# Performance work log

Measured on AMD Instinct MI355X. Metric: run time of the kernel, lower is better.

The kernel has to match this reference:

```python
import jax, jax.numpy as jnp
import numpy as np

NCLASSES = 1000
K = 5
REG_STRENGTH = 1.0


def isotonic_l2(y):
    """Solve min_v 0.5||v - y||^2 s.t. v_1 >= v_2 >= ... >= v_n, per row.

    Uses the exact min-max characterization of isotonic regression:
      sol_i = min_{j<=i} max_{k>=i} mean(y[j..k])
    (equivalent to pool-adjacent-violators), fully vectorized.
    y: [B, n] -> [B, n]
    """
    b, n = y.shape
    cs = jnp.concatenate([jnp.zeros((b, 1), y.dtype), jnp.cumsum(y, axis=-1)], axis=-1)  # [B, n+1]
    j = jnp.arange(n)[:, None]  # block start
    k = jnp.arange(n)[None, :]  # block end
    length = (k - j + 1).astype(y.dtype)
    # M[b, j, k] = mean(y[b, j..k]) for k >= j, else -inf (ignored by the max)
    M = (cs[:, None, 1:] - cs[:, :-1, None]) / jnp.where(k >= j, length, 1.0)
    M = jnp.where(k >= j, M, -jnp.inf)
    A = jax.lax.cummax(M, axis=2, reverse=True)  # A[b, j, i] = max_{k>=i} M[b, j, k]
    A = jnp.where(j <= k, A, jnp.inf)            # restrict min to j <= i
    return jnp.min(A, axis=1)                     # [B, n]


def soft_rank(values, strength):
    """torchsort.soft_rank with l2 regularization.

    r = theta - sigma^{-1}(isotonic_l2(sort_desc(theta) - w)),  theta = values/strength,
    w = [n, n-1, ..., 1].  Larger values get larger (soft) ranks.
    """
    n = values.shape[-1]
    theta = values / strength
    perm = jnp.argsort(-theta, axis=-1)                 # descending order
    s = jnp.take_along_axis(theta, perm, axis=-1)
    inv_perm = jnp.argsort(perm, axis=-1)
    w = jnp.arange(n, 0, -1, dtype=values.dtype)
    sol = isotonic_l2(s - w[None, :])
    return jnp.take_along_axis(s - sol, inv_perm, axis=-1)


def setup_inputs() -> dict:
    key = jax.random.key(0)
    k1, k2 = jax.random.split(key)
    output = jax.random.normal(k1, (64, NCLASSES), dtype=jnp.float32)
    target = jax.random.randint(k2, (64,), 0, NCLASSES, dtype=jnp.int32)
    return {"output": output, "target": target}


def reference(output, target):
    ranks = soft_rank(output, REG_STRENGTH)                              # [B, n]
    ranks_label = jnp.take_along_axis(ranks, target[:, None], axis=-1)   # [B, 1]
    return jnp.mean(jax.nn.relu(NCLASSES - ranks_label - K + 1))
```

## Files before the change

kernel.cpp:

```cpp
#include <hip/hip_runtime.h>
#include <math.h>

#define N     1000
#define NPAD  1024
#define NTH1  512
#define NTH2  256
#define MSLICE 16
#define SROW  1040
#define META  (64 * SROW)

__device__ inline unsigned fkey(float x) {
    unsigned u = __float_as_uint(x);
    return (u & 0x80000000u) ? ~u : (u | 0x80000000u);
}
__device__ inline float fdecode(unsigned u) {
    return __uint_as_float((u & 0x80000000u) ? (u & 0x7FFFFFFFu) : ~u);
}

__global__ __launch_bounds__(NTH1) void k1_sort_scan(
    const float* __restrict__ mat, const int* __restrict__ target,
    float* __restrict__ ws)
{
    __shared__ float sx[NPAD];
    __shared__ float wtot[8];
    __shared__ int   cnt_sh;

    const int tid  = threadIdx.x;
    const int lane = tid & 63;
    const int w    = tid >> 6;
    const int i0   = (w << 7) + lane;
    const int i1   = i0 + 64;
    const int r    = blockIdx.x;
    const float* row = mat + r * N;
    const int   tgt  = target[r];
    const float tval = row[tgt];

    float r0 = row[i0];
    float r1 = (i1 < N) ? row[i1] : -INFINITY;
    if (tid == 0) cnt_sh = 0;

    int lc = ((r0 > tval) || (r0 == tval && i0 < tgt))
           + ((r1 > tval) || (r1 == tval && i1 < tgt));
    #pragma unroll
    for (int off = 32; off; off >>= 1) lc += __shfl_down(lc, off);
    __syncthreads();
    if (lane == 0 && lc) atomicAdd(&cnt_sh, lc);

    auto cas_shfl = [&](float& rr, int i, unsigned k, unsigned j) {
        float o = __shfl_xor(rr, (int)j);
        bool lower = ((lane & (int)j) == 0);
        bool desc  = ((i & (int)k) == 0);
        rr = (lower == desc) ? fmaxf(rr, o) : fminf(rr, o);
    };
    #pragma unroll
    for (unsigned k = 2; k <= 64; k <<= 1)
        #pragma unroll
        for (unsigned j = k >> 1; j; j >>= 1) { cas_shfl(r0, i0, k, j); cas_shfl(r1, i1, k, j); }
    #pragma unroll
    for (unsigned k = 128; k <= 1024; k <<= 1) {
        #pragma unroll
        for (unsigned j = k >> 1; j >= 128; j >>= 1) {
            __syncthreads();
            sx[i0] = r0; sx[i1] = r1;
            __syncthreads();
            float o0 = sx[i0 ^ (int)j], o1 = sx[i1 ^ (int)j];
            bool lower = ((i0 & (int)j) == 0);
            bool desc  = ((i0 & (int)k) == 0);
            r0 = (lower == desc) ? fmaxf(r0, o0) : fminf(r0, o0);
            r1 = (lower == desc) ? fmaxf(r1, o1) : fminf(r1, o1);
        }
        {
            bool desc = ((i0 & (int)k) == 0);
            float a = fmaxf(r0, r1), b = fminf(r0, r1);
            r0 = desc ? a : b;
            r1 = desc ? b : a;
        }
        #pragma unroll
        for (unsigned j = 32; j; j >>= 1) { cas_shfl(r0, i0, k, j); cas_shfl(r1, i1, k, j); }
    }

    if (i1 >= N) r1 = 0.0f;
    float incl0 = r0;
    #pragma unroll
    for (int off = 1; off < 64; off <<= 1) {
        float y = __shfl_up(incl0, off);
        if (lane >= off) incl0 += y;
    }
    float tot0 = __shfl(incl0, 63);
    float incl1 = r1;
    #pragma unroll
    for (int off = 1; off < 64; off <<= 1) {
        float y = __shfl_up(incl1, off);
        if (lane >= off) incl1 += y;
    }
    if (lane == 63) wtot[w] = incl0 + incl1;
    __syncthreads();
    float base = 0.0f;
    #pragma unroll
    for (int u = 0; u < 8; ++u) { float t = wtot[u]; if (u < w) base += t; }

    float* Sg = ws + r * SROW;
    if (tid == 0) Sg[0] = 0.0f;
    Sg[i0 + 1] = base + incl0;
    Sg[i1 + 1] = base + tot0 + incl1;
    if (tid == 0) {
        ((int*)ws)[META + r]            = cnt_sh;
        ws[META + 64 + r]               = tval;
        ((unsigned*)ws)[META + 128 + r] = 0xFFFFFFFFu;
    }
}

__global__ __launch_bounds__(NTH2) void k2_minmax(
    const float* __restrict__ Sg, const int* __restrict__ pw,
    unsigned* __restrict__ mr)
{
    __shared__ float Sloc[N];
    __shared__ float rtab[N];
    __shared__ float maxh[NTH2];

    const int r  = blockIdx.y;
    const int m  = blockIdx.x;
    const int t  = threadIdx.x;
    const int p  = pw[r];
    const int j0 = m * 64;
    if (j0 > p) return;
    const int len = N - p;
    const float* Srow = Sg + r * SROW;

    const int jl = t & 63;
    const int j  = j0 + jl;
    const float Sj = (j <= p) ? Srow[j] : 0.0f;

    for (int i = t; i < len; i += NTH2) Sloc[i] = Srow[p + 1 + i];
    for (int d = t; d < N; d += NTH2) rtab[d] = 1.0f / (float)(d + 1);
    __syncthreads();

    const int q  = t >> 6;
    const int k0 = (q * len) >> 2;
    const int k1 = ((q + 1) * len) >> 2;
    float maxv = -INFINITY;
    if (j <= p) {
        const float* sp = &Sloc[k0];
        const float* rp = &rtab[p + k0 - j];
        float c = 0.5f * (float)(j + p + k0) - (float)N;
        #pragma unroll 8
        for (int it = 0; it < k1 - k0; ++it) {
            float mval = fmaf(sp[it] - Sj, rp[it], c);
            maxv = fmaxf(maxv, mval);
            c += 0.5f;
        }
    }
    maxh[t] = maxv;
    __syncthreads();
    if (t < 64) {
        float mv = fmaxf(fmaxf(maxh[t], maxh[t + 64]),
                         fmaxf(maxh[t + 128], maxh[t + 192]));
        float minv = (j0 + t <= p) ? mv : INFINITY;
        #pragma unroll
        for (int off = 32; off; off >>= 1)
            minv = fminf(minv, __shfl_down(minv, off));
        if (t == 0) atomicMin(&mr[r], fkey(minv));
    }
}

__global__ __launch_bounds__(64) void k3_loss(
    const unsigned* __restrict__ mr, const float* __restrict__ tv,
    float* __restrict__ out, int nrows)
{
    int t = threadIdx.x;
    float loss = 0.0f;
    if (t < nrows) {
        float sol  = fdecode(mr[t]);
        float rank = tv[t] - sol;
        loss = fmaxf(0.0f, (float)(N - 5 + 1) - rank);
    }
    #pragma unroll
    for (int off = 32; off; off >>= 1) loss += __shfl_down(loss, off);
    if (t == 0) out[0] = loss / (float)nrows;
}

__global__ __launch_bounds__(NTH1) void topk_loss_mono(
    const float* __restrict__ mat, const int* __restrict__ target,
    float* __restrict__ d_out, int nrows)
{
    __shared__ float S[NPAD + 1];
    __shared__ float rcp[N];
    __shared__ float sx[NPAD];
    __shared__ float wtot[8];
    __shared__ float red[8];
    __shared__ int   cnt_sh;

    const int tid  = threadIdx.x;
    const int lane = tid & 63;
    const int w    = tid >> 6;
    const int i0   = (w << 7) + lane;
    const int i1   = i0 + 64;
    const float* row = mat + blockIdx.x * N;
    const int   tgt  = target[blockIdx.x];
    const float tval = row[tgt];

    float r0 = row[i0];
    float r1 = (i1 < N) ? row[i1] : -INFINITY;
    if (tid == 0) cnt_sh = 0;
    rcp[tid] = 1.0f / (float)(tid + 1);
    if (tid + NTH1 < N) rcp[tid + NTH1] = 1.0f / (float)(tid + NTH1 + 1);

    int lc = ((r0 > tval) || (r0 == tval && i0 < tgt))
           + ((r1 > tval) || (r1 == tval && i1 < tgt));
    #pragma unroll
    for (int off = 32; off; off >>= 1) lc += __shfl_down(lc, off);
    __syncthreads();
    if (lane == 0 && lc) atomicAdd(&cnt_sh, lc);

    auto cas_shfl = [&](float& rr, int i, unsigned k, unsigned j) {
        float o = __shfl_xor(rr, (int)j);
        bool lower = ((lane & (int)j) == 0);
        bool desc  = ((i & (int)k) == 0);
        rr = (lower == desc) ? fmaxf(rr, o) : fminf(rr, o);
    };
    #pragma unroll
    for (unsigned k = 2; k <= 64; k <<= 1)
        #pragma unroll
        for (unsigned j = k >> 1; j; j >>= 1) { cas_shfl(r0, i0, k, j); cas_shfl(r1, i1, k, j); }
    #pragma unroll
    for (unsigned k = 128; k <= 1024; k <<= 1) {
        #pragma unroll
        for (unsigned j = k >> 1; j >= 128; j >>= 1) {
            __syncthreads();
            sx[i0] = r0; sx[i1] = r1;
            __syncthreads();
            float o0 = sx[i0 ^ (int)j], o1 = sx[i1 ^ (int)j];
            bool lower = ((i0 & (int)j) == 0);
            bool desc  = ((i0 & (int)k) == 0);
            r0 = (lower == desc) ? fmaxf(r0, o0) : fminf(r0, o0);
            r1 = (lower == desc) ? fmaxf(r1, o1) : fminf(r1, o1);
        }
        {
            bool desc = ((i0 & (int)k) == 0);
            float a = fmaxf(r0, r1), b = fminf(r0, r1);
            r0 = desc ? a : b;
            r1 = desc ? b : a;
        }
        #pragma unroll
        for (unsigned j = 32; j; j >>= 1) { cas_shfl(r0, i0, k, j); cas_shfl(r1, i1, k, j); }
    }

    if (i1 >= N) r1 = 0.0f;
    float incl0 = r0;
    #pragma unroll
    for (int off = 1; off < 64; off <<= 1) {
        float y = __shfl_up(incl0, off);
        if (lane >= off) incl0 += y;
    }
    float tot0 = __shfl(incl0, 63);
    float incl1 = r1;
    #pragma unroll
    for (int off = 1; off < 64; off <<= 1) {
        float y = __shfl_up(incl1, off);
        if (lane >= off) incl1 += y;
    }
    if (lane == 63) wtot[w] = incl0 + incl1;
    __syncthreads();
    float base = 0.0f;
    #pragma unroll
    for (int u = 0; u < 8; ++u) { float t = wtot[u]; if (u < w) base += t; }
    if (tid == 0) S[0] = 0.0f;
    S[i0 + 1] = base + incl0;
    S[i1 + 1] = base + tot0 + incl1;
    __syncthreads();

    const int p   = cnt_sh;
    const int len = N - p;
    float minv = INFINITY;
    for (int j = tid; j <= p; j += NTH1) {
        const float  Sj = S[j];
        const float* Sp = &S[p + 1];
        const float* rp = &rcp[p - j];
        const float  cj = 0.5f * (float)(j + p) - (float)N;
        float maxv = -INFINITY;
        #pragma unroll 8
        for (int it = 0; it < len; ++it) {
            float mm = fmaf(Sp[it] - Sj, rp[it], cj + 0.5f * (float)it);
            maxv = fmaxf(maxv, mm);
        }
        minv = fminf(minv, maxv);
    }
    #pragma unroll
    for (int off = 32; off; off >>= 1) minv = fminf(minv, __shfl_down(minv, off));
    if (lane == 0) red[w] = minv;
    __syncthreads();
    if (tid == 0) {
        float sol = red[0];
        #pragma unroll
        for (int u = 1; u < 8; ++u) sol = fminf(sol, red[u]);
        float rank_label = tval - sol;
        float loss = fmaxf(0.0f, (float)(N - 5 + 1) - rank_label);
        atomicAdd(d_out, loss / (float)nrows);
    }
}

extern "C" void kernel_launch(void* const* d_in, const int* in_sizes, int n_in,
                              void* d_out, int out_size, void* d_ws, size_t ws_size,
                              hipStream_t stream) {
    (void)n_in;
    const float* mat    = (const float*)d_in[0];
    const int*   target = (const int*)d_in[1];
    float*       out    = (float*)d_out;
    const int    nrows  = in_sizes[1];

    const size_t need = (size_t)(META + 192) * sizeof(float);
    if (nrows == 64 && ws_size >= need) {
        float*    ws = (float*)d_ws;
        float*    Sg = ws;
        int*      pw = (int*)(ws + META);
        float*    tv = ws + META + 64;
        unsigned* mr = (unsigned*)(ws + META + 128);
        k1_sort_scan<<<nrows, NTH1, 0, stream>>>(mat, target, ws);
        dim3 g2(MSLICE, nrows);
        k2_minmax<<<g2, NTH2, 0, stream>>>(Sg, pw, mr);
        k3_loss<<<1, 64, 0, stream>>>(mr, tv, out, nrows);
    } else {
        hipMemsetAsync(out, 0, sizeof(float) * out_size, stream);
        topk_loss_mono<<<nrows, NTH1, 0, stream>>>(mat, target, out, nrows);
    }
}
```

Baseline: 70.31 us.

## Fuse final loss kernel into minmax via last-block atomic counter; double-buffer sort

Removes the third kernel launch. The final loss reduction now runs in whichever k2 block is last to increment a global done-counter, which k1 resets. The block-wide bitonic stages in k1 use a double-buffered shared array, cutting one __syncthreads per stage. This trades a launch and a barrier per stage for an extra atomic and a threadfence in every k2 block.

```diff
diff --git a/kernel.cpp b/kernel.cpp
--- a/kernel.cpp
+++ b/kernel.cpp
@@ -1,13 +1,13 @@
 #include <hip/hip_runtime.h>
 #include <math.h>
 
-#define N     1000
-#define NPAD  1024
-#define NTH1  512
-#define NTH2  256
+#define N      1000
+#define NTH1   512
+#define NTH2   256
 #define MSLICE 16
-#define SROW  1040
-#define META  (64 * SROW)
+#define SROW   1008
+#define META   (64 * SROW)
+#define K2_BLOCKS (MSLICE * 64)
 
 __device__ inline unsigned fkey(float x) {
     unsigned u = __float_as_uint(x);
@@ -21,7 +21,7 @@
     const float* __restrict__ mat, const int* __restrict__ target,
     float* __restrict__ ws)
 {
-    __shared__ float sx[NPAD];
+    __shared__ float sx[2][1024];
     __shared__ float wtot[8];
     __shared__ int   cnt_sh;
 
@@ -56,14 +56,15 @@
     for (unsigned k = 2; k <= 64; k <<= 1)
         #pragma unroll
         for (unsigned j = k >> 1; j; j >>= 1) { cas_shfl(r0, i0, k, j); cas_shfl(r1, i1, k, j); }
+    int buf = 0;
     #pragma unroll
     for (unsigned k = 128; k <= 1024; k <<= 1) {
         #pragma unroll
         for (unsigned j = k >> 1; j >= 128; j >>= 1) {
+            sx[buf][i0] = r0; sx[buf][i1] = r1;
             __syncthreads();
-            sx[i0] = r0; sx[i1] = r1;
-            __syncthreads();
-            float o0 = sx[i0 ^ (int)j], o1 = sx[i1 ^ (int)j];
+            float o0 = sx[buf][i0 ^ (int)j], o1 = sx[buf][i1 ^ (int)j];
+            buf ^= 1;
             bool lower = ((i0 & (int)j) == 0);
             bool desc  = ((i0 & (int)k) == 0);
             r0 = (lower == desc) ? fmaxf(r0, o0) : fminf(r0, o0);
@@ -102,90 +103,92 @@
     float* Sg = ws + r * SROW;
     if (tid == 0) Sg[0] = 0.0f;
     Sg[i0 + 1] = base + incl0;
-    Sg[i1 + 1] = base + tot0 + incl1;
+    if (i1 < N) Sg[i1 + 1] = base + tot0 + incl1;
     if (tid == 0) {
         ((int*)ws)[META + r]            = cnt_sh;
         ws[META + 64 + r]               = tval;
         ((unsigned*)ws)[META + 128 + r] = 0xFFFFFFFFu;
+        if (r == 0) ((unsigned*)ws)[META + 192] = 0u;
     }
 }
 
 __global__ __launch_bounds__(NTH2) void k2_minmax(
-    const float* __restrict__ Sg, const int* __restrict__ pw,
-    unsigned* __restrict__ mr)
+    float* __restrict__ ws, float* __restrict__ out)
 {
     __shared__ float Sloc[N];
     __shared__ float rtab[N];
     __shared__ float maxh[NTH2];
+    __shared__ int   amLast;
 
     const int r  = blockIdx.y;
     const int m  = blockIdx.x;
     const int t  = threadIdx.x;
-    const int p  = pw[r];
+    const int p  = ((const int*)ws)[META + r];
     const int j0 = m * 64;
-    if (j0 > p) return;
-    const int len = N - p;
-    const float* Srow = Sg + r * SROW;
-
-    const int jl = t & 63;
-    const int j  = j0 + jl;
-    const float Sj = (j <= p) ? Srow[j] : 0.0f;
-
-    for (int i = t; i < len; i += NTH2) Sloc[i] = Srow[p + 1 + i];
-    for (int d = t; d < N; d += NTH2) rtab[d] = 1.0f / (float)(d + 1);
-    __syncthreads();
-
-    const int q  = t >> 6;
-    const int k0 = (q * len) >> 2;
-    const int k1 = ((q + 1) * len) >> 2;
-    float maxv = -INFINITY;
-    if (j <= p) {
-        const float* sp = &Sloc[k0];
-        const float* rp = &rtab[p + k0 - j];
-        float c = 0.5f * (float)(j + p + k0) - (float)N;
-        #pragma unroll 8
-        for (int it = 0; it < k1 - k0; ++it) {
-            float mval = fmaf(sp[it] - Sj, rp[it], c);
-            maxv = fmaxf(maxv, mval);
-            c += 0.5f;
-        }
-    }
-    maxh[t] = maxv;
-    __syncthreads();
-    if (t < 64) {
-        float mv = fmaxf(fmaxf(maxh[t], maxh[t + 64]),
-                         fmaxf(maxh[t + 128], maxh[t + 192]));
-        float minv = (j0 + t <= p) ? mv : INFINITY;
-        #pragma unroll
-        for (int off = 32; off; off >>= 1)
-            minv = fminf(minv, __shfl_down(minv, off));
-        if (t == 0) atomicMin(&mr[r], fkey(minv));
-    }
-}
-
-__global__ __launch_bounds__(64) void k3_loss(
-    const unsigned* __restrict__ mr, const float* __restrict__ tv,
-    float* __restrict__ out, int nrows)
-{
-    int t = threadIdx.x;
-    float loss = 0.0f;
-    if (t < nrows) {
-        float sol  = fdecode(mr[t]);
-        float rank = tv[t] - sol;
-        loss = fmaxf(0.0f, (float)(N - 5 + 1) - rank);
-    }
-    #pragma unroll
-    for (int off = 32; off; off >>= 1) loss += __shfl_down(loss, off);
-    if (t == 0) out[0] = loss / (float)nrows;
+    unsigned* mr   = (unsigned*)ws + META + 128;
+    unsigned* done = (unsigned*)ws + META + 192;
+
+    if (j0 <= p) {
+        const int len = N - p;
+        const float* Srow = ws + r * SROW;
+        const int jl = t & 63;
+        const int j  = j0 + jl;
+        const float Sj = (j <= p) ? Srow[j] : 0.0f;
+
+        for (int i = t; i < len; i += NTH2) Sloc[i] = Srow[p + 1 + i];
+        for (int d = t; d < N; d += NTH2) rtab[d] = 1.0f / (float)(d + 1);
+        __syncthreads();
+
+        const int q  = t >> 6;
+        const int k0 = (q * len) >> 2;
+        const int k1 = ((q + 1) * len) >> 2;
+        float maxv = -INFINITY;
+        if (j <= p) {
+            const float* sp = &Sloc[k0];
+            const float* rp = &rtab[p + k0 - j];
+            float c = 0.5f * (float)(j + p + k0) - (float)N;
+            #pragma unroll 8
+            for (int it = 0; it < k1 - k0; ++it) {
+                float mval = fmaf(sp[it] - Sj, rp[it], c);
+                maxv = fmaxf(maxv, mval);
+                c += 0.5f;
+            }
+        }
+        maxh[t] = maxv;
+        __syncthreads();
+        if (t < 64) {
+            float mv = fmaxf(fmaxf(maxh[t], maxh[t + 64]),
+                             fmaxf(maxh[t + 128], maxh[t + 192]));
+            float minv = (j0 + t <= p) ? mv : INFINITY;
+            #pragma unroll
+            for (int off = 32; off; off >>= 1)
+                minv = fminf(minv, __shfl_down(minv, off));
+            if (t == 0) atomicMin(&mr[r], fkey(minv));
+        }
+    }
+
+    if (t == 0) {
+        __threadfence();
+        amLast = (atomicAdd(done, 1u) == K2_BLOCKS - 1);
+    }
+    __syncthreads();
+    if (amLast && t < 64) {
+        float sol  = fdecode(atomicAdd(&mr[t], 0u));
+        float tval = ws[META + 64 + t];
+        float loss = fmaxf(0.0f, (float)(N - 5 + 1) - (tval - sol));
+        #pragma unroll
+        for (int off = 32; off; off >>= 1) loss += __shfl_down(loss, off);
+        if (t == 0) out[0] = loss / 64.0f;
+    }
 }
 
 __global__ __launch_bounds__(NTH1) void topk_loss_mono(
     const float* __restrict__ mat, const int* __restrict__ target,
     float* __restrict__ d_out, int nrows)
 {
-    __shared__ float S[NPAD + 1];
+    __shared__ float S[1025];
     __shared__ float rcp[N];
-    __shared__ float sx[NPAD];
+    __shared__ float sx[1024];
     __shared__ float wtot[8];
     __shared__ float red[8];
     __shared__ int   cnt_sh;
@@ -308,17 +311,12 @@
     float*       out    = (float*)d_out;
     const int    nrows  = in_sizes[1];
 
-    const size_t need = (size_t)(META + 192) * sizeof(float);
+    const size_t need = (size_t)(META + 256) * sizeof(float);
     if (nrows == 64 && ws_size >= need) {
-        float*    ws = (float*)d_ws;
-        float*    Sg = ws;
-        int*      pw = (int*)(ws + META);
-        float*    tv = ws + META + 64;
-        unsigned* mr = (unsigned*)(ws + META + 128);
+        float* ws = (float*)d_ws;
         k1_sort_scan<<<nrows, NTH1, 0, stream>>>(mat, target, ws);
         dim3 g2(MSLICE, nrows);
-        k2_minmax<<<g2, NTH2, 0, stream>>>(Sg, pw, mr);
-        k3_loss<<<1, 64, 0, stream>>>(mr, tv, out, nrows);
+        k2_minmax<<<g2, NTH2, 0, stream>>>(ws, out);
     } else {
         hipMemsetAsync(out, 0, sizeof(float) * out_size, stream);
         topk_loss_mono<<<nrows, NTH1, 0, stream>>>(mat, target, out, nrows);
```

Result: slower. 79.33 us (+12.8%).
